# Performance work log

Measured on AMD Instinct MI355X. Metric: run time of the kernel, lower is better.

Reference implementation:

```python
import jax, jax.numpy as jnp
import numpy as np

N = 50000   # nodes
E = 800000  # edges (no self-loops; self-loops added in forward)
B = 128     # graphs
EPS = 1e-16  # PyG softmax denominator epsilon


def _gat(x, W, a_src, a_dst, bias, src, dst, heads, C, concat):
    n = x.shape[0]
    xp = (x @ W).reshape(n, heads, C)                      # [N,H,C]
    s_src = (xp * a_src).sum(-1)                           # [N,H]
    s_dst = (xp * a_dst).sum(-1)                           # [N,H]
    alpha = jax.nn.leaky_relu(s_src[src] + s_dst[dst], 0.2)  # [E',H]
    m = jax.ops.segment_max(alpha, dst, num_segments=n)
    ex = jnp.exp(alpha - m[dst])
    den = jax.ops.segment_sum(ex, dst, num_segments=n) + EPS
    a = ex / den[dst]                                      # edge softmax over in-edges
    out = jax.ops.segment_sum(a[:, :, None] * xp[src], dst, num_segments=n)  # [N,H,C]
    out = out.reshape(n, heads * C) if concat else out.mean(axis=1)
    return out + bias


def _forward(x, edge_attr, W1, b1, ln_g, ln_b, W2, b2,
             Wg1, as1, ad1, bg1, Wg2, as2, ad2, bg2, Wg3, as3, ad3, bg3,
             Wih, Whh, bih, bhh, edge_index, batch):
    # feature encoder: Linear -> LayerNorm -> LeakyReLU(0.1) -> Linear (dropout: eval mode)
    h = x @ W1 + b1
    mu = h.mean(-1, keepdims=True)
    var = ((h - mu) ** 2).mean(-1, keepdims=True)
    h = (h - mu) / jnp.sqrt(var + 1e-5) * ln_g + ln_b
    h = jax.nn.leaky_relu(h, 0.1)
    h = h @ W2 + b2                                        # [N,256]
    # add self loops once (edge_attr is unused: edge_dim=None => lin_edge is None)
    sl = jnp.arange(N, dtype=edge_index.dtype)
    src = jnp.concatenate([edge_index[0], sl])
    dst = jnp.concatenate([edge_index[1], sl])
    g = _gat(h, Wg1, as1, ad1, bg1, src, dst, 2, 64, True)   # [N,128]
    g = jax.nn.leaky_relu(g, 0.1)
    g = _gat(g, Wg2, as2, ad2, bg2, src, dst, 2, 64, True)   # [N,128]
    g = jax.nn.elu(g)
    g = _gat(g, Wg3, as3, ad3, bg3, src, dst, 1, 64, False)  # [N,64]
    # Set2Set(64, processing_steps=5)
    q_star = jnp.zeros((B, 128), g.dtype)
    hS = jnp.zeros((B, 64), g.dtype)
    cS = jnp.zeros((B, 64), g.dtype)
    for _ in range(5):
        gates = q_star @ Wih.T + bih + hS @ Whh.T + bhh      # [B,256]
        i, f, gg, o = jnp.split(gates, 4, axis=-1)
        cS = jax.nn.sigmoid(f) * cS + jax.nn.sigmoid(i) * jnp.tanh(gg)
        hS = jax.nn.sigmoid(o) * jnp.tanh(cS)                # q = h [B,64]
        e = (g * hS[batch]).sum(-1)                          # [N]
        m = jax.ops.segment_max(e, batch, num_segments=B)
        a = jnp.exp(e - m[batch])
        a = a / (jax.ops.segment_sum(a, batch, num_segments=B) + EPS)[batch]
        r = jax.ops.segment_sum(a[:, None] * g, batch, num_segments=B)  # [B,64]
        q_star = jnp.concatenate([hS, r], axis=-1)
    return q_star  # [B,128]


def setup_inputs():
    key = jax.random.key(0)
    ks = jax.random.split(key, 32)
    nrm = lambda k, sh, s=0.1: (jax.random.normal(k, sh) * s).astype(jnp.float32)
    src = jax.random.randint(ks[0], (E,), 0, N, dtype=jnp.int32)
    off = jax.random.randint(ks[1], (E,), 1, N, dtype=jnp.int32)
    dst = (src + off) % N  # no self-loops
    edge_index = jnp.stack([src, dst])
    batch = jnp.sort(jax.random.randint(ks[2], (N,), 0, B, dtype=jnp.int32))
    return dict(
        x=jax.random.normal(ks[3], (N, 6), jnp.float32),
        edge_index=edge_index,
        edge_attr=jax.random.normal(ks[4], (E, 4), jnp.float32),
        batch=batch,
        W1=nrm(ks[5], (6, 128)), b1=jnp.zeros((128,), jnp.float32),
        ln_g=jnp.ones((128,), jnp.float32), ln_b=jnp.zeros((128,), jnp.float32),
        W2=nrm(ks[6], (128, 256)), b2=jnp.zeros((256,), jnp.float32),
        Wg1=nrm(ks[7], (256, 128)), as1=nrm(ks[8], (2, 64)), ad1=nrm(ks[9], (2, 64)), bg1=jnp.zeros((128,), jnp.float32),
        Wg2=nrm(ks[10], (128, 128)), as2=nrm(ks[11], (2, 64)), ad2=nrm(ks[12], (2, 64)), bg2=jnp.zeros((128,), jnp.float32),
        Wg3=nrm(ks[13], (128, 64)), as3=nrm(ks[14], (1, 64)), ad3=nrm(ks[15], (1, 64)), bg3=jnp.zeros((64,), jnp.float32),
        Wih=nrm(ks[16], (256, 128)), Whh=nrm(ks[17], (256, 64)),
        bih=jnp.zeros((256,), jnp.float32), bhh=jnp.zeros((256,), jnp.float32),
    )


def reference(x, edge_index, edge_attr, batch, W1, b1, ln_g, ln_b, W2, b2,
              Wg1, as1, ad1, bg1, Wg2, as2, ad2, bg2, Wg3, as3, ad3, bg3,
              Wih, Whh, bih, bhh):
    return _forward(x, edge_attr, W1, b1, ln_g, ln_b, W2, b2,
                    Wg1, as1, ad1, bg1, Wg2, as2, ad2, bg2, Wg3, as3, ad3, bg3,
                    Wih, Whh, bih, bhh, edge_index, batch)
```

## Files before the change

### kernel.cpp

```cpp
#include <hip/hip_runtime.h>
#include <hip/hip_bf16.h>
#include <math.h>

#define N_NODES 50000
#define M_PAD   50176
#define N_EDGES 800000
#define N_B     128
#define EPRIME  (N_EDGES + N_NODES)
#define NBUCKETS 196
#define CCHUNK  8192
#define NCHUNKS ((EPRIME + CCHUNK - 1) / CCHUNK)
#define ENC_B   ((N_NODES + 3) / 4)
#define WT_B    (90112 / 256)
#define S2S_MAXN 512
#define GEMME_B  1564
#define GEMM1_B  782

typedef __attribute__((ext_vector_type(8))) short bf16x8;
typedef __attribute__((ext_vector_type(4))) float f32x4;
typedef unsigned short ushort_t;

__device__ __forceinline__ float sigmoidf_(float x) { return 1.f / (1.f + __expf(-x)); }

__device__ __forceinline__ void wtr1(const float* W, __hip_bfloat16* Wt, int K, int N, int i) {
    int k = i / N, n = i - k * N;
    Wt[(size_t)n * K + k] = __float2bfloat16(W[i]);
}

__global__ __launch_bounds__(256) void prep_k(
        const float* __restrict__ x, const float* __restrict__ W1,
        const float* __restrict__ b1, const float* __restrict__ lng,
        const float* __restrict__ lnb, __hip_bfloat16* __restrict__ h1,
        const float* __restrict__ W2, const float* __restrict__ Wg1,
        const float* __restrict__ Wg2, const float* __restrict__ Wg3,
        __hip_bfloat16* W2t, __hip_bfloat16* Wg1t,
        __hip_bfloat16* Wg2t, __hip_bfloat16* Wg3t,
        const int* __restrict__ e_dst, int* __restrict__ bpart) {
    int blk = blockIdx.x;
    if (blk < ENC_B) {
        int w = (blk * 256 + threadIdx.x) >> 6;
        int lane = threadIdx.x & 63;
        if (w >= N_NODES) return;
        float xr[6];
#pragma unroll
        for (int k = 0; k < 6; ++k) xr[k] = x[w * 6 + k];
        float a = b1[lane], b = b1[lane + 64];
#pragma unroll
        for (int k = 0; k < 6; ++k) {
            a += xr[k] * W1[k * 128 + lane];
            b += xr[k] * W1[k * 128 + 64 + lane];
        }
        float s = a + b, s2 = a * a + b * b;
        for (int o = 32; o; o >>= 1) { s += __shfl_xor(s, o); s2 += __shfl_xor(s2, o); }
        float mu  = s * (1.f / 128.f);
        float var = s2 * (1.f / 128.f) - mu * mu;
        float inv = rsqrtf(var + 1e-5f);
        a = (a - mu) * inv * lng[lane] + lnb[lane];
        b = (b - mu) * inv * lng[lane + 64] + lnb[lane + 64];
        a = a > 0.f ? a : 0.1f * a;
        b = b > 0.f ? b : 0.1f * b;
        h1[(size_t)w * 128 + lane]      = __float2bfloat16(a);
        h1[(size_t)w * 128 + 64 + lane] = __float2bfloat16(b);
    } else if (blk < ENC_B + WT_B) {
        int i = (blk - ENC_B) * 256 + threadIdx.x;
        if (i < 32768)       wtr1(W2,  W2t,  128, 256, i);
        else if (i < 65536)  wtr1(Wg1, Wg1t, 256, 128, i - 32768);
        else if (i < 81920)  wtr1(Wg2, Wg2t, 128, 128, i - 65536);
        else                 wtr1(Wg3, Wg3t, 128, 64,  i - 81920);
    } else {
        __shared__ int h[NBUCKETS];
        int c = blk - ENC_B - WT_B;
        for (int i = threadIdx.x; i < NBUCKETS; i += 256) h[i] = 0;
        __syncthreads();
        int base = c * CCHUNK;
        int end = min(base + CCHUNK, EPRIME);
        for (int e = base + threadIdx.x; e < end; e += 256) {
            int d = (e < N_EDGES) ? e_dst[e] : (e - N_EDGES);
            atomicAdd(&h[d >> 8], 1);
        }
        __syncthreads();
        for (int i = threadIdx.x; i < NBUCKETS; i += 256)
            bpart[c * NBUCKETS + i] = h[i];
    }
}

__global__ __launch_bounds__(256) void scan2_k(const int* __restrict__ bpart,
        int* __restrict__ boff, int* __restrict__ cpre) {
    __shared__ int sm[256];
    int t = threadIdx.x;
    int run = 0;
    if (t < NBUCKETS) {
        for (int j = 0; j < NCHUNKS; ++j) {
            cpre[j * NBUCKETS + t] = run;
            run += bpart[j * NBUCKETS + t];
        }
    }
    sm[t] = run; __syncthreads();
    for (int o = 1; o < 256; o <<= 1) {
        int xv = (t >= o) ? sm[t - o] : 0;
        __syncthreads();
        sm[t] += xv;
        __syncthreads();
    }
    int excl = sm[t] - run;
    if (t < NBUCKETS) boff[t] = excl;
    if (t == NBUCKETS - 1) boff[NBUCKETS] = excl + run;
}

__device__ __forceinline__ void partition_body(int c, const int* __restrict__ e_src,
        const int* __restrict__ e_dst, const int* __restrict__ boff,
        const int* __restrict__ cpre, int* __restrict__ epack,
        int* h2, int* gbase) {
    for (int i = threadIdx.x; i < NBUCKETS; i += 256) {
        h2[i] = 0;
        gbase[i] = boff[i] + cpre[c * NBUCKETS + i];
    }
    __syncthreads();
    int base = c * CCHUNK;
    int end = min(base + CCHUNK, EPRIME);
    for (int e = base + threadIdx.x; e < end; e += 256) {
        int s, d;
        if (e < N_EDGES) { s = e_src[e]; d = e_dst[e]; }
        else             { s = e - N_EDGES; d = s; }
        int b = d >> 8;
        int rank = atomicAdd(&h2[b], 1);
        epack[gbase[b] + rank] = ((d & 255) << 16) | s;
    }
}

__device__ __forceinline__ void csr_build_body(int b, const int* __restrict__ epack,
        const int* __restrict__ boff, int* __restrict__ off,
        ushort_t* __restrict__ csr, int* deg, int* cur, int* sm) {
    int t = threadIdx.x;
    int gb0 = boff[b];
    int gcnt = boff[b + 1] - gb0;
    deg[t] = 0;
    __syncthreads();
    for (int i = t; i < gcnt; i += 256)
        atomicAdd(&deg[(epack[gb0 + i] >> 16) & 0xFF], 1);
    __syncthreads();
    int v = deg[t];
    sm[t] = v; __syncthreads();
    for (int o = 1; o < 256; o <<= 1) {
        int xv = (t >= o) ? sm[t - o] : 0;
        __syncthreads();
        sm[t] += xv;
        __syncthreads();
    }
    int excl = sm[t] - v;
    int idx = b * 256 + t;
    if (idx <= N_NODES) off[idx] = gb0 + excl;
    cur[t] = gb0 + excl;
    __syncthreads();
    for (int i = t; i < gcnt; i += 256) {
        int pk = epack[gb0 + i];
        int ld = (pk >> 16) & 0xFF;
        int pos = atomicAdd(&cur[ld], 1);
        csr[pos] = (ushort_t)(pk & 0xFFFF);
    }
}

template<int K, int N, int BM, int BN, int WN, bool BIAS, int SDH>
__device__ __forceinline__ void mfma_body(short* As, float* sdbuf, int bx, int by,
        const __hip_bfloat16* __restrict__ A, const __hip_bfloat16* __restrict__ Wt,
        const float* __restrict__ bias, void* __restrict__ Cv,
        const float* __restrict__ asrc, const float* __restrict__ adst,
        float* __restrict__ ssrc, float* __restrict__ sdst, int M) {
    constexpr int KT = K / 32;
    constexpr int NISSUE = BM / 64;
    const int tid  = threadIdx.x;
    const int wid  = tid >> 6;
    const int lane = tid & 63;
    const int wm = wid / WN;
    const int wn = wid % WN;
    const int row0 = by * BM;
    const int col0 = bx * BN + wn * 32;

    if (SDH > 0) {
        for (int i = tid; i < BM * SDH * 2; i += 256) sdbuf[i] = 0.f;
    }

    bf16x8 breg[KT][2];
#pragma unroll
    for (int kt = 0; kt < KT; ++kt)
#pragma unroll
        for (int cb = 0; cb < 2; ++cb) {
            int col = col0 + cb * 16 + (lane & 15);
            int k   = kt * 32 + (lane >> 4) * 8;
            breg[kt][cb] = *(const bf16x8*)&Wt[(size_t)col * K + k];
        }

    f32x4 acc[4][2];
#pragma unroll
    for (int rb = 0; rb < 4; ++rb)
#pragma unroll
        for (int cb = 0; cb < 2; ++cb) acc[rb][cb] = f32x4{0.f, 0.f, 0.f, 0.f};

    int4 rbuf[NISSUE];
#pragma unroll
    for (int is = 0; is < NISSUE; ++is) {
        int lr = is * 64 + wid * 16 + (lane >> 2);
        rbuf[is] = *(const int4*)&A[(size_t)(row0 + lr) * K + (lane & 3) * 8];
    }
#pragma unroll
    for (int kt = 0; kt < KT; ++kt) {
        if (kt) __syncthreads();
#pragma unroll
        for (int is = 0; is < NISSUE; ++is) {
            int lr   = is * 64 + wid * 16 + (lane >> 2);
            int slot = (lane & 3) ^ ((lr >> 1) & 3);
            *(int4*)((char*)As + lr * 64 + slot * 16) = rbuf[is];
        }
        if (kt + 1 < KT) {
#pragma unroll
            for (int is = 0; is < NISSUE; ++is) {
                int lr = is * 64 + wid * 16 + (lane >> 2);
                rbuf[is] = *(const int4*)&A[(size_t)(row0 + lr) * K +
                                            (kt + 1) * 32 + (lane & 3) * 8];
            }
        }
        __syncthreads();
        bf16x8 af[4];
#pragma unroll
        for (int rb = 0; rb < 4; ++rb) {
            int row  = wm * 64 + rb * 16 + (lane & 15);
            int slot = (lane >> 4) ^ ((row >> 1) & 3);
            af[rb] = *(const bf16x8*)((char*)As + row * 64 + slot * 16);
        }
#pragma unroll
        for (int rb = 0; rb < 4; ++rb)
#pragma unroll
            for (int cb = 0; cb < 2; ++cb)
                acc[rb][cb] = __builtin_amdgcn_mfma_f32_16x16x32_bf16(
                    af[rb], breg[kt][cb], acc[rb][cb], 0, 0, 0);
    }

    if (SDH > 0) {
        float av0 = asrc[col0 + (lane & 15)],       ad0 = adst[col0 + (lane & 15)];
        float av1 = asrc[col0 + 16 + (lane & 15)],  ad1 = adst[col0 + 16 + (lane & 15)];
        int h = (SDH == 2) ? (wn >> 1) : 0;
#pragma unroll
        for (int rb = 0; rb < 4; ++rb) {
#pragma unroll
            for (int r = 0; r < 4; ++r) {
                float ssv = acc[rb][0][r] * av0 + acc[rb][1][r] * av1;
                float sdv = acc[rb][0][r] * ad0 + acc[rb][1][r] * ad1;
#pragma unroll
                for (int o = 1; o < 16; o <<= 1) {
                    ssv += __shfl_xor(ssv, o);
                    sdv += __shfl_xor(sdv, o);
                }
                if ((lane & 15) == 0) {
                    int rl = wm * 64 + rb * 16 + (lane >> 4) * 4 + r;
                    atomicAdd(&sdbuf[(rl * SDH + h) * 2 + 0], ssv);
                    atomicAdd(&sdbuf[(rl * SDH + h) * 2 + 1], sdv);
                }
            }
        }
        __syncthreads();
        if (tid < BM) {
            int row = row0 + tid;
            if (row < M) {
                if (SDH == 2) {
                    ((float2*)ssrc)[row] = make_float2(sdbuf[(tid * 2 + 0) * 2 + 0],
                                                       sdbuf[(tid * 2 + 1) * 2 + 0]);
                    ((float2*)sdst)[row] = make_float2(sdbuf[(tid * 2 + 0) * 2 + 1],
                                                       sdbuf[(tid * 2 + 1) * 2 + 1]);
                } else {
                    ssrc[row] = sdbuf[tid * 2 + 0];
                    sdst[row] = sdbuf[tid * 2 + 1];
                }
            }
        }
    }

#pragma unroll
    for (int rb = 0; rb < 4; ++rb) {
        int rowb = row0 + wm * 64 + rb * 16 + (lane >> 4) * 4;
#pragma unroll
        for (int cb = 0; cb < 2; ++cb) {
            int col = col0 + cb * 16 + (lane & 15);
            float bval = BIAS ? bias[col] : 0.f;
#pragma unroll
            for (int r = 0; r < 4; ++r) {
                int row = rowb + r;
                if (row < M) {
                    float v = acc[rb][cb][r] + bval;
                    ((__hip_bfloat16*)Cv)[(size_t)row * N + col] = __float2bfloat16(v);
                }
            }
        }
    }
}

__global__ __launch_bounds__(256) void gemmE_part_k(
        const __hip_bfloat16* __restrict__ A, const __hip_bfloat16* __restrict__ Wt,
        const float* __restrict__ bias, __hip_bfloat16* __restrict__ C,
        const int* __restrict__ e_src, const int* __restrict__ e_dst,
        const int* __restrict__ boff, const int* __restrict__ cpre,
        int* __restrict__ epack) {
    __shared__ short As[64 * 32];
    __shared__ int h2[NBUCKETS], gbase[NBUCKETS];
    int blk = blockIdx.x;
    if (blk < GEMME_B) {
        mfma_body<128, 256, 64, 128, 4, true, 0>(As, nullptr, blk & 1, blk >> 1,
            A, Wt, bias, C, nullptr, nullptr, nullptr, nullptr, N_NODES);
    } else {
        partition_body(blk - GEMME_B, e_src, e_dst, boff, cpre, epack, h2, gbase);
    }
}

__global__ __launch_bounds__(256) void gemm1_csr_k(
        const __hip_bfloat16* __restrict__ A, const __hip_bfloat16* __restrict__ Wt,
        __hip_bfloat16* __restrict__ C,
        const float* __restrict__ asrc, const float* __restrict__ adst,
        float* __restrict__ ssrc, float* __restrict__ sdst,
        const int* __restrict__ epack, const int* __restrict__ boff,
        int* __restrict__ off, ushort_t* __restrict__ csr) {
    __shared__ short As[64 * 32];
    __shared__ float sdbuf[64 * 2 * 2];
    __shared__ int deg[256], cur[256], sm[256];
    int blk = blockIdx.x;
    if (blk < GEMM1_B) {
        mfma_body<256, 128, 64, 128, 4, false, 2>(As, sdbuf, 0, blk,
            A, Wt, nullptr, C, asrc, adst, ssrc, sdst, N_NODES);
    } else {
        csr_build_body(blk - GEMM1_B, epack, boff, off, csr, deg, cur, sm);
    }
}

template<int K, int N, int BM, int BN, int WN, int SDH>
__global__ __launch_bounds__(256) void gemm_k(
        const __hip_bfloat16* __restrict__ A, const __hip_bfloat16* __restrict__ Wt,
        __hip_bfloat16* __restrict__ C,
        const float* __restrict__ asrc, const float* __restrict__ adst,
        float* __restrict__ ssrc, float* __restrict__ sdst) {
    __shared__ short As[BM * 32];
    __shared__ float sdbuf[SDH > 0 ? BM * SDH * 2 : 1];
    mfma_body<K, N, BM, BN, WN, false, SDH>(As, sdbuf, 0, blockIdx.x,
        A, Wt, nullptr, C, asrc, adst, ssrc, sdst, N_NODES);
}

template<int ACT>
__global__ __launch_bounds__(256) void gat_agg2_k(const __hip_bfloat16* __restrict__ xp,
        const float2* __restrict__ s_src2, const float2* __restrict__ s_dst2,
        const int* __restrict__ off, const ushort_t* __restrict__ csr_src,
        const float* __restrict__ bias, __hip_bfloat16* __restrict__ outb) {
    int n = (blockIdx.x * 256 + threadIdx.x) >> 6;
    int lane = threadIdx.x & 63;
    if (n >= N_NODES) return;
    const float2 sdn = s_dst2[n];
    const int i0 = off[n];
    const int deg = off[n + 1] - i0;
    const unsigned* __restrict__ xprow = (const unsigned*)xp;
    float accx = 0.f, accy = 0.f;
    float d0 = 0.f, d1 = 0.f;
    for (int c0 = 0; c0 < deg; c0 += 64) {
        int cnt = min(64, deg - c0);
        int se = 0; float e0 = 0.f, e1 = 0.f;
        if (lane < cnt) {
            se = csr_src[i0 + c0 + lane];
            float2 ssv = s_src2[se];
            float a0 = ssv.x + sdn.x; a0 = a0 > 0.f ? a0 : 0.2f * a0;
            float a1 = ssv.y + sdn.y; a1 = a1 > 0.f ? a1 : 0.2f * a1;
            e0 = __expf(a0); e1 = __expf(a1);
        }
        d0 += e0; d1 += e1;
        unsigned e0u = __float_as_uint(e0), e1u = __float_as_uint(e1);
        int e = 0;
        for (; e + 4 <= cnt; e += 4) {
            int s0 = __builtin_amdgcn_readlane(se, e + 0);
            int s1 = __builtin_amdgcn_readlane(se, e + 1);
            int s2 = __builtin_amdgcn_readlane(se, e + 2);
            int s3 = __builtin_amdgcn_readlane(se, e + 3);
            unsigned w0 = xprow[((unsigned)s0 << 6) + lane];
            unsigned w1 = xprow[((unsigned)s1 << 6) + lane];
            unsigned w2 = xprow[((unsigned)s2 << 6) + lane];
            unsigned w3 = xprow[((unsigned)s3 << 6) + lane];
            float p00 = __uint_as_float(__builtin_amdgcn_readlane(e0u, e + 0));
            float p01 = __uint_as_float(__builtin_amdgcn_readlane(e1u, e + 0));
            float p10 = __uint_as_float(__builtin_amdgcn_readlane(e0u, e + 1));
            float p11 = __uint_as_float(__builtin_amdgcn_readlane(e1u, e + 1));
            float p20 = __uint_as_float(__builtin_amdgcn_readlane(e0u, e + 2));
            float p21 = __uint_as_float(__builtin_amdgcn_readlane(e1u, e + 2));
            float p30 = __uint_as_float(__builtin_amdgcn_readlane(e0u, e + 3));
            float p31 = __uint_as_float(__builtin_amdgcn_readlane(e1u, e + 3));
            float q0 = lane < 32 ? p00 : p01;
            float q1 = lane < 32 ? p10 : p11;
            float q2 = lane < 32 ? p20 : p21;
            float q3 = lane < 32 ? p30 : p31;
            accx += q0 * __uint_as_float(w0 << 16);
            accy += q0 * __uint_as_float(w0 & 0xffff0000u);
            accx += q1 * __uint_as_float(w1 << 16);
            accy += q1 * __uint_as_float(w1 & 0xffff0000u);
            accx += q2 * __uint_as_float(w2 << 16);
            accy += q2 * __uint_as_float(w2 & 0xffff0000u);
            accx += q3 * __uint_as_float(w3 << 16);
            accy += q3 * __uint_as_float(w3 & 0xffff0000u);
        }
        for (; e < cnt; ++e) {
            int s = __builtin_amdgcn_readlane(se, e);
            unsigned w = xprow[((unsigned)s << 6) + lane];
            float p0 = __uint_as_float(__builtin_amdgcn_readlane(e0u, e));
            float p1 = __uint_as_float(__builtin_amdgcn_readlane(e1u, e));
            float q = lane < 32 ? p0 : p1;
            accx += q * __uint_as_float(w << 16);
            accy += q * __uint_as_float(w & 0xffff0000u);
        }
    }
    for (int o = 32; o; o >>= 1) { d0 += __shfl_xor(d0, o); d1 += __shfl_xor(d1, o); }
    float den = (lane < 32 ? d0 : d1) + 1e-16f;
    float2 bv = ((const float2*)bias)[lane];
    float r0 = accx / den + bv.x;
    float r1 = accy / den + bv.y;
    if (ACT == 1) { r0 = r0 > 0.f ? r0 : 0.1f * r0; r1 = r1 > 0.f ? r1 : 0.1f * r1; }
    else          { r0 = r0 > 0.f ? r0 : (__expf(r0) - 1.f);
                    r1 = r1 > 0.f ? r1 : (__expf(r1) - 1.f); }
    __hip_bfloat16 h0 = __float2bfloat16(r0), h1v = __float2bfloat16(r1);
    unsigned packed = (unsigned)*(unsigned short*)&h0 |
                      ((unsigned)*(unsigned short*)&h1v << 16);
    ((unsigned*)outb)[(size_t)n * 64 + lane] = packed;
}

__global__ __launch_bounds__(256) void gat_agg1_k(const __hip_bfloat16* __restrict__ xp,
        const float* __restrict__ s_src, const float* __restrict__ s_dst,
        const int* __restrict__ off, const ushort_t* __restrict__ csr_src,
        const float* __restrict__ bias, float* __restrict__ out) {
    int n = (blockIdx.x * 256 + threadIdx.x) >> 6;
    int lane = threadIdx.x & 63;
    if (n >= N_NODES) return;
    const float sdn = s_dst[n];
    const int i0 = off[n];
    const int deg = off[n + 1] - i0;
    float acc = 0.f, d0 = 0.f;
    for (int c0 = 0; c0 < deg; c0 += 64) {
        int cnt = min(64, deg - c0);
        int se = 0; float ev = 0.f;
        if (lane < cnt) {
            se = csr_src[i0 + c0 + lane];
            float a = s_src[se] + sdn;
            a = a > 0.f ? a : 0.2f * a;
            ev = __expf(a);
        }
        d0 += ev;
        unsigned evu = __float_as_uint(ev);
        int e = 0;
        for (; e + 4 <= cnt; e += 4) {
            int s0 = __builtin_amdgcn_readlane(se, e + 0);
            int s1 = __builtin_amdgcn_readlane(se, e + 1);
            int s2 = __builtin_amdgcn_readlane(se, e + 2);
            int s3 = __builtin_amdgcn_readlane(se, e + 3);
            float w0 = __uint_as_float(__builtin_amdgcn_readlane(evu, e + 0));
            float w1 = __uint_as_float(__builtin_amdgcn_readlane(evu, e + 1));
            float w2 = __uint_as_float(__builtin_amdgcn_readlane(evu, e + 2));
            float w3 = __uint_as_float(__builtin_amdgcn_readlane(evu, e + 3));
            acc += w0 * __bfloat162float(xp[((unsigned)s0 << 6) + lane]);
            acc += w1 * __bfloat162float(xp[((unsigned)s1 << 6) + lane]);
            acc += w2 * __bfloat162float(xp[((unsigned)s2 << 6) + lane]);
            acc += w3 * __bfloat162float(xp[((unsigned)s3 << 6) + lane]);
        }
        for (; e < cnt; ++e) {
            int s = __builtin_amdgcn_readlane(se, e);
            float w = __uint_as_float(__builtin_amdgcn_readlane(evu, e));
            acc += w * __bfloat162float(xp[((unsigned)s << 6) + lane]);
        }
    }
    for (int o = 32; o; o >>= 1) d0 += __shfl_xor(d0, o);
    out[(size_t)n * 64 + lane] = acc / (d0 + 1e-16f) + bias[lane];
}

__global__ __launch_bounds__(512) void s2s_fused_k(const float* __restrict__ g3,
        const int* __restrict__ batch,
        const float* __restrict__ Wih, const float* __restrict__ Whh,
        const float* __restrict__ bih, const float* __restrict__ bhh,
        float* __restrict__ out) {
    __shared__ __align__(16) float g3L[S2S_MAXN * 68];
    __shared__ float p_sh[S2S_MAXN];
    __shared__ __align__(16) float hsh[64];
    __shared__ float q[128], csh[64], gates[256];
    __shared__ float rred[8][64];
    __shared__ float dred[8];
    __shared__ int sn0, sn1;
    int b = blockIdx.x;
    int t = threadIdx.x;
    int lane = t & 63, wv = t >> 6;
    if (t == 0) {
        int lo = 0, hi = N_NODES;
        while (lo < hi) { int mid = (lo + hi) >> 1; if (batch[mid] < b) lo = mid + 1; else hi = mid; }
        sn0 = lo;
        lo = 0; hi = N_NODES;
        while (lo < hi) { int mid = (lo + hi) >> 1; if (batch[mid] < b + 1) lo = mid + 1; else hi = mid; }
        sn1 = lo;
    }
    if (t < 128) q[t] = 0.f;
    if (t < 64) { hsh[t] = 0.f; csh[t] = 0.f; }
    __syncthreads();
    const int n0 = sn0;
    const int cnt = min(sn1 - sn0, S2S_MAXN);
    for (int i = t; i < cnt * 16; i += 512) {
        int r = i >> 4, c4 = i & 15;
        ((float4*)&g3L[r * 68])[c4] = ((const float4*)(g3 + ((size_t)(n0 + r) << 6)))[c4];
    }
    __syncthreads();
    for (int step = 0; step < 5; ++step) {
        if (t < 256) {
            float g = bih[t] + bhh[t];
            const float4* wi4 = (const float4*)(Wih + (size_t)t * 128);
#pragma unroll 8
            for (int k4 = 0; k4 < 32; ++k4) {
                float4 w = wi4[k4];
                g += q[k4 * 4 + 0] * w.x + q[k4 * 4 + 1] * w.y +
                     q[k4 * 4 + 2] * w.z + q[k4 * 4 + 3] * w.w;
            }
            const float4* wh4 = (const float4*)(Whh + (size_t)t * 64);
#pragma unroll 8
            for (int k4 = 0; k4 < 16; ++k4) {
                float4 w = wh4[k4];
                g += hsh[k4 * 4 + 0] * w.x + hsh[k4 * 4 + 1] * w.y +
                     hsh[k4 * 4 + 2] * w.z + hsh[k4 * 4 + 3] * w.w;
            }
            gates[t] = g;
        }
        __syncthreads();
        if (t < 64) {
            float iv = sigmoidf_(gates[t]);
            float fv = sigmoidf_(gates[64 + t]);
            float gv = tanhf(gates[128 + t]);
            float ov = sigmoidf_(gates[192 + t]);
            float c = fv * csh[t] + iv * gv;
            csh[t] = c;
            hsh[t] = ov * tanhf(c);
        }
        __syncthreads();
        float4 hr[16];
#pragma unroll
        for (int k = 0; k < 16; ++k) hr[k] = ((const float4*)hsh)[k];
        for (int base = 0; base < cnt; base += 512) {
            int n = base + t;
            if (n < cnt) {
                const float4* row = (const float4*)&g3L[n * 68];
                float a0 = 0.f, a1 = 0.f, a2 = 0.f, a3 = 0.f;
#pragma unroll
                for (int k = 0; k < 16; k += 4) {
                    float4 r0 = row[k], r1 = row[k + 1], r2 = row[k + 2], r3 = row[k + 3];
                    a0 += r0.x * hr[k].x + r0.y * hr[k].y + r0.z * hr[k].z + r0.w * hr[k].w;
                    a1 += r1.x * hr[k+1].x + r1.y * hr[k+1].y + r1.z * hr[k+1].z + r1.w * hr[k+1].w;
                    a2 += r2.x * hr[k+2].x + r2.y * hr[k+2].y + r2.z * hr[k+2].z + r2.w * hr[k+2].w;
                    a3 += r3.x * hr[k+3].x + r3.y * hr[k+3].y + r3.z * hr[k+3].z + r3.w * hr[k+3].w;
                }
                p_sh[n] = __expf((a0 + a1) + (a2 + a3));
            }
        }
        __syncthreads();
        float rloc = 0.f, dloc = 0.f;
        int n = wv;
        for (; n + 8 < cnt; n += 16) {
            float pv0 = p_sh[n], pv1 = p_sh[n + 8];
            float gv0 = g3L[n * 68 + lane], gv1 = g3L[(n + 8) * 68 + lane];
            dloc += pv0 + pv1;
            rloc += pv0 * gv0 + pv1 * gv1;
        }
        if (n < cnt) {
            float pv = p_sh[n];
            float gv = g3L[n * 68 + lane];
            dloc += pv; rloc += pv * gv;
        }
        rred[wv][lane] = rloc;
        if (lane == 0) dred[wv] = dloc;
        __syncthreads();
        if (t < 64) {
            float r = rred[0][t] + rred[1][t] + rred[2][t] + rred[3][t] +
                      rred[4][t] + rred[5][t] + rred[6][t] + rred[7][t];
            float den = dred[0] + dred[1] + dred[2] + dred[3] +
                        dred[4] + dred[5] + dred[6] + dred[7] + 1e-16f;
            q[t] = hsh[t];
            q[64 + t] = r / den;
        }
        __syncthreads();
    }
    if (t < 128) out[b * 128 + t] = q[t];
}

extern "C" void kernel_launch(void* const* d_in, const int* in_sizes, int n_in,
                              void* d_out, int out_size, void* d_ws, size_t ws_size,
                              hipStream_t stream) {
    (void)in_sizes; (void)n_in; (void)out_size; (void)ws_size;
    const float* x     = (const float*)d_in[0];
    const int*   ei    = (const int*)d_in[1];
    const int*   batch = (const int*)d_in[3];
    const float* W1  = (const float*)d_in[4];
    const float* b1  = (const float*)d_in[5];
    const float* lng = (const float*)d_in[6];
    const float* lnb = (const float*)d_in[7];
    const float* W2  = (const float*)d_in[8];
    const float* b2  = (const float*)d_in[9];
    const float* Wg1 = (const float*)d_in[10];
    const float* as1 = (const float*)d_in[11];
    const float* ad1 = (const float*)d_in[12];
    const float* bg1 = (const float*)d_in[13];
    const float* Wg2 = (const float*)d_in[14];
    const float* as2 = (const float*)d_in[15];
    const float* ad2 = (const float*)d_in[16];
    const float* bg2 = (const float*)d_in[17];
    const float* Wg3 = (const float*)d_in[18];
    const float* as3 = (const float*)d_in[19];
    const float* ad3 = (const float*)d_in[20];
    const float* bg3 = (const float*)d_in[21];
    const float* Wih = (const float*)d_in[22];
    const float* Whh = (const float*)d_in[23];
    const float* bih = (const float*)d_in[24];
    const float* bhh = (const float*)d_in[25];
    const int* e_src = ei;
    const int* e_dst = ei + N_EDGES;
    float* out = (float*)d_out;

    char* p = (char*)d_ws;
    auto carve = [&](size_t bytes) {
        char* r = p;
        p += (bytes + 255) & ~(size_t)255;
        return r;
    };
    __hip_bfloat16* actA = (__hip_bfloat16*)carve((size_t)M_PAD * 256 * 2);
    __hip_bfloat16* actB = (__hip_bfloat16*)carve((size_t)M_PAD * 128 * 2);
    __hip_bfloat16* actC = (__hip_bfloat16*)carve((size_t)M_PAD * 128 * 2);
    float* g3     = (float*)carve((size_t)M_PAD * 64 * 4);
    float* s_src  = (float*)carve((size_t)N_NODES * 2 * 4);
    float* s_dst  = (float*)carve((size_t)N_NODES * 2 * 4);
    int*   off    = (int*)carve((size_t)(N_NODES + 1) * 4);
    int*   epack  = (int*)carve((size_t)EPRIME * 4);
    ushort_t* csr = (ushort_t*)carve((size_t)EPRIME * 2);
    int*   bpart  = (int*)carve((size_t)NCHUNKS * NBUCKETS * 4);
    int*   cpre   = (int*)carve((size_t)NCHUNKS * NBUCKETS * 4);
    int*   boff   = (int*)carve((NBUCKETS + 1) * 4);
    __hip_bfloat16* W2t  = (__hip_bfloat16*)carve(256 * 128 * 2);
    __hip_bfloat16* Wg1t = (__hip_bfloat16*)carve(128 * 256 * 2);
    __hip_bfloat16* Wg2t = (__hip_bfloat16*)carve(128 * 128 * 2);
    __hip_bfloat16* Wg3t = (__hip_bfloat16*)carve(64 * 128 * 2);

    dim3 blk(256);

    prep_k<<<ENC_B + WT_B + NCHUNKS, blk, 0, stream>>>(
        x, W1, b1, lng, lnb, actB,
        W2, Wg1, Wg2, Wg3, W2t, Wg1t, Wg2t, Wg3t,
        e_dst, bpart);

    scan2_k<<<1, blk, 0, stream>>>(bpart, boff, cpre);

    gemmE_part_k<<<GEMME_B + NCHUNKS, blk, 0, stream>>>(
        actB, W2t, b2, actA, e_src, e_dst, boff, cpre, epack);

    gemm1_csr_k<<<GEMM1_B + NBUCKETS, blk, 0, stream>>>(
        actA, Wg1t, actB, as1, ad1, s_src, s_dst, epack, boff, off, csr);
    gat_agg2_k<1><<<(N_NODES + 3) / 4, blk, 0, stream>>>(
        actB, (const float2*)s_src, (const float2*)s_dst, off, csr, bg1, actC);

    gemm_k<128, 128, 64, 128, 4, 2><<<GEMM1_B, blk, 0, stream>>>(
        actC, Wg2t, actB, as2, ad2, s_src, s_dst);
    gat_agg2_k<2><<<(N_NODES + 3) / 4, blk, 0, stream>>>(
        actB, (const float2*)s_src, (const float2*)s_dst, off, csr, bg2, actC);

    gemm_k<128, 64, 128, 64, 2, 1><<<391, blk, 0, stream>>>(
        actC, Wg3t, actB, as3, ad3, s_src, s_dst);
    gat_agg1_k<<<(N_NODES + 3) / 4, blk, 0, stream>>>(
        actB, s_src, s_dst, off, csr, bg3, g3);

    s2s_fused_k<<<N_B, dim3(512), 0, stream>>>(g3, batch, Wih, Whh, bih, bhh, out);
}
```

Measured before the change: 398.2 us.

## Gather neighbor rows with 16-byte loads per edge group and transpose LSTM weights

```diff
diff --git a/kernel.cpp b/kernel.cpp
--- a/kernel.cpp
+++ b/kernel.cpp
@@ -11,7 +11,8 @@
 #define CCHUNK  8192
 #define NCHUNKS ((EPRIME + CCHUNK - 1) / CCHUNK)
 #define ENC_B   ((N_NODES + 3) / 4)
-#define WT_B    (90112 / 256)
+#define WT_ELEMS (90112 + 32768 + 16384)
+#define WT_B    ((WT_ELEMS + 255) / 256)
 #define S2S_MAXN 512
 #define GEMME_B  1564
 #define GEMM1_B  782
@@ -35,6 +36,8 @@
         const float* __restrict__ Wg2, const float* __restrict__ Wg3,
         __hip_bfloat16* W2t, __hip_bfloat16* Wg1t,
         __hip_bfloat16* Wg2t, __hip_bfloat16* Wg3t,
+        const float* __restrict__ Wih, const float* __restrict__ Whh,
+        float* __restrict__ WihT, float* __restrict__ WhhT,
         const int* __restrict__ e_dst, int* __restrict__ bpart) {
     int blk = blockIdx.x;
     if (blk < ENC_B) {
@@ -66,7 +69,16 @@
         if (i < 32768)       wtr1(W2,  W2t,  128, 256, i);
         else if (i < 65536)  wtr1(Wg1, Wg1t, 256, 128, i - 32768);
         else if (i < 81920)  wtr1(Wg2, Wg2t, 128, 128, i - 65536);
-        else                 wtr1(Wg3, Wg3t, 128, 64,  i - 81920);
+        else if (i < 90112)  wtr1(Wg3, Wg3t, 128, 64,  i - 81920);
+        else if (i < 122880) {
+            int ii = i - 90112;
+            int k = ii >> 8, j = ii & 255;
+            WihT[ii] = Wih[(size_t)j * 128 + k];
+        } else if (i < WT_ELEMS) {
+            int ii = i - 122880;
+            int k = ii >> 8, j = ii & 255;
+            WhhT[ii] = Whh[(size_t)j * 64 + k];
+        }
     } else {
         __shared__ int h[NBUCKETS];
         int c = blk - ENC_B - WT_B;
@@ -349,12 +361,15 @@
     int n = (blockIdx.x * 256 + threadIdx.x) >> 6;
     int lane = threadIdx.x & 63;
     if (n >= N_NODES) return;
+    const int grp = lane >> 4;
+    const int slot = lane & 15;
     const float2 sdn = s_dst2[n];
     const int i0 = off[n];
     const int deg = off[n + 1] - i0;
-    const unsigned* __restrict__ xprow = (const unsigned*)xp;
-    float accx = 0.f, accy = 0.f;
+    const int4* __restrict__ xprow4 = (const int4*)xp;
+    float acc[8] = {0.f, 0.f, 0.f, 0.f, 0.f, 0.f, 0.f, 0.f};
     float d0 = 0.f, d1 = 0.f;
+    const int bbase = grp << 2;
     for (int c0 = 0; c0 < deg; c0 += 64) {
         int cnt = min(64, deg - c0);
         int se = 0; float e0 = 0.f, e1 = 0.f;
@@ -366,60 +381,54 @@
             e0 = __expf(a0); e1 = __expf(a1);
         }
         d0 += e0; d1 += e1;
-        unsigned e0u = __float_as_uint(e0), e1u = __float_as_uint(e1);
-        int e = 0;
-        for (; e + 4 <= cnt; e += 4) {
-            int s0 = __builtin_amdgcn_readlane(se, e + 0);
-            int s1 = __builtin_amdgcn_readlane(se, e + 1);
-            int s2 = __builtin_amdgcn_readlane(se, e + 2);
-            int s3 = __builtin_amdgcn_readlane(se, e + 3);
-            unsigned w0 = xprow[((unsigned)s0 << 6) + lane];
-            unsigned w1 = xprow[((unsigned)s1 << 6) + lane];
-            unsigned w2 = xprow[((unsigned)s2 << 6) + lane];
-            unsigned w3 = xprow[((unsigned)s3 << 6) + lane];
-            float p00 = __uint_as_float(__builtin_amdgcn_readlane(e0u, e + 0));
-            float p01 = __uint_as_float(__builtin_amdgcn_readlane(e1u, e + 0));
-            float p10 = __uint_as_float(__builtin_amdgcn_readlane(e0u, e + 1));
-            float p11 = __uint_as_float(__builtin_amdgcn_readlane(e1u, e + 1));
-            float p20 = __uint_as_float(__builtin_amdgcn_readlane(e0u, e + 2));
-            float p21 = __uint_as_float(__builtin_amdgcn_readlane(e1u, e + 2));
-            float p30 = __uint_as_float(__builtin_amdgcn_readlane(e0u, e + 3));
-            float p31 = __uint_as_float(__builtin_amdgcn_readlane(e1u, e + 3));
-            float q0 = lane < 32 ? p00 : p01;
-            float q1 = lane < 32 ? p10 : p11;
-            float q2 = lane < 32 ? p20 : p21;
-            float q3 = lane < 32 ? p30 : p31;
-            accx += q0 * __uint_as_float(w0 << 16);
-            accy += q0 * __uint_as_float(w0 & 0xffff0000u);
-            accx += q1 * __uint_as_float(w1 << 16);
-            accy += q1 * __uint_as_float(w1 & 0xffff0000u);
-            accx += q2 * __uint_as_float(w2 << 16);
-            accy += q2 * __uint_as_float(w2 & 0xffff0000u);
-            accx += q3 * __uint_as_float(w3 << 16);
-            accy += q3 * __uint_as_float(w3 & 0xffff0000u);
-        }
-        for (; e < cnt; ++e) {
-            int s = __builtin_amdgcn_readlane(se, e);
-            unsigned w = xprow[((unsigned)s << 6) + lane];
-            float p0 = __uint_as_float(__builtin_amdgcn_readlane(e0u, e));
-            float p1 = __uint_as_float(__builtin_amdgcn_readlane(e1u, e));
-            float q = lane < 32 ? p0 : p1;
-            accx += q * __uint_as_float(w << 16);
-            accy += q * __uint_as_float(w & 0xffff0000u);
-        }
+        int e0i = __float_as_int(e0), e1i = __float_as_int(e1);
+        for (int e = 0; e < cnt; e += 4) {
+            int bidx = (e << 2) + bbase;
+            int s  = __builtin_amdgcn_ds_bpermute(bidx, se);
+            float w0 = __int_as_float(__builtin_amdgcn_ds_bpermute(bidx, e0i));
+            float w1 = __int_as_float(__builtin_amdgcn_ds_bpermute(bidx, e1i));
+            float qv = slot < 8 ? w0 : w1;
+            int4 row = xprow4[(size_t)s * 16 + slot];
+            acc[0] += qv * __uint_as_float((unsigned)row.x << 16);
+            acc[1] += qv * __uint_as_float((unsigned)row.x & 0xffff0000u);
+            acc[2] += qv * __uint_as_float((unsigned)row.y << 16);
+            acc[3] += qv * __uint_as_float((unsigned)row.y & 0xffff0000u);
+            acc[4] += qv * __uint_as_float((unsigned)row.z << 16);
+            acc[5] += qv * __uint_as_float((unsigned)row.z & 0xffff0000u);
+            acc[6] += qv * __uint_as_float((unsigned)row.w << 16);
+            acc[7] += qv * __uint_as_float((unsigned)row.w & 0xffff0000u);
+        }
+    }
+#pragma unroll
+    for (int j = 0; j < 8; ++j) {
+        acc[j] += __shfl_xor(acc[j], 16);
+        acc[j] += __shfl_xor(acc[j], 32);
     }
     for (int o = 32; o; o >>= 1) { d0 += __shfl_xor(d0, o); d1 += __shfl_xor(d1, o); }
-    float den = (lane < 32 ? d0 : d1) + 1e-16f;
-    float2 bv = ((const float2*)bias)[lane];
-    float r0 = accx / den + bv.x;
-    float r1 = accy / den + bv.y;
-    if (ACT == 1) { r0 = r0 > 0.f ? r0 : 0.1f * r0; r1 = r1 > 0.f ? r1 : 0.1f * r1; }
-    else          { r0 = r0 > 0.f ? r0 : (__expf(r0) - 1.f);
-                    r1 = r1 > 0.f ? r1 : (__expf(r1) - 1.f); }
-    __hip_bfloat16 h0 = __float2bfloat16(r0), h1v = __float2bfloat16(r1);
-    unsigned packed = (unsigned)*(unsigned short*)&h0 |
-                      ((unsigned)*(unsigned short*)&h1v << 16);
-    ((unsigned*)outb)[(size_t)n * 64 + lane] = packed;
+    if (grp == 0) {
+        float den = (slot < 8 ? d0 : d1) + 1e-16f;
+        float4 bv0 = ((const float4*)bias)[slot * 2];
+        float4 bv1 = ((const float4*)bias)[slot * 2 + 1];
+        float r[8];
+        r[0] = acc[0] / den + bv0.x; r[1] = acc[1] / den + bv0.y;
+        r[2] = acc[2] / den + bv0.z; r[3] = acc[3] / den + bv0.w;
+        r[4] = acc[4] / den + bv1.x; r[5] = acc[5] / den + bv1.y;
+        r[6] = acc[6] / den + bv1.z; r[7] = acc[7] / den + bv1.w;
+#pragma unroll
+        for (int j = 0; j < 8; ++j) {
+            if (ACT == 1) r[j] = r[j] > 0.f ? r[j] : 0.1f * r[j];
+            else          r[j] = r[j] > 0.f ? r[j] : (__expf(r[j]) - 1.f);
+        }
+        int pk[4];
+#pragma unroll
+        for (int j = 0; j < 4; ++j) {
+            __hip_bfloat16 lo = __float2bfloat16(r[2 * j]);
+            __hip_bfloat16 hi = __float2bfloat16(r[2 * j + 1]);
+            pk[j] = (int)(unsigned)*(unsigned short*)&lo |
+                    ((int)(unsigned)*(unsigned short*)&hi << 16);
+        }
+        ((int4*)outb)[(size_t)n * 16 + slot] = make_int4(pk[0], pk[1], pk[2], pk[3]);
+    }
 }
 
 __global__ __launch_bounds__(256) void gat_agg1_k(const __hip_bfloat16* __restrict__ xp,
@@ -429,10 +438,15 @@
     int n = (blockIdx.x * 256 + threadIdx.x) >> 6;
     int lane = threadIdx.x & 63;
     if (n >= N_NODES) return;
+    const int grp = lane >> 3;
+    const int slot = lane & 7;
     const float sdn = s_dst[n];
     const int i0 = off[n];
     const int deg = off[n + 1] - i0;
-    float acc = 0.f, d0 = 0.f;
+    const int4* __restrict__ xprow4 = (const int4*)xp;
+    float acc[8] = {0.f, 0.f, 0.f, 0.f, 0.f, 0.f, 0.f, 0.f};
+    float d0 = 0.f;
+    const int bbase = grp << 2;
     for (int c0 = 0; c0 < deg; c0 += 64) {
         int cnt = min(64, deg - c0);
         int se = 0; float ev = 0.f;
@@ -443,41 +457,52 @@
             ev = __expf(a);
         }
         d0 += ev;
-        unsigned evu = __float_as_uint(ev);
-        int e = 0;
-        for (; e + 4 <= cnt; e += 4) {
-            int s0 = __builtin_amdgcn_readlane(se, e + 0);
-            int s1 = __builtin_amdgcn_readlane(se, e + 1);
-            int s2 = __builtin_amdgcn_readlane(se, e + 2);
-            int s3 = __builtin_amdgcn_readlane(se, e + 3);
-            float w0 = __uint_as_float(__builtin_amdgcn_readlane(evu, e + 0));
-            float w1 = __uint_as_float(__builtin_amdgcn_readlane(evu, e + 1));
-            float w2 = __uint_as_float(__builtin_amdgcn_readlane(evu, e + 2));
-            float w3 = __uint_as_float(__builtin_amdgcn_readlane(evu, e + 3));
-            acc += w0 * __bfloat162float(xp[((unsigned)s0 << 6) + lane]);
-            acc += w1 * __bfloat162float(xp[((unsigned)s1 << 6) + lane]);
-            acc += w2 * __bfloat162float(xp[((unsigned)s2 << 6) + lane]);
-            acc += w3 * __bfloat162float(xp[((unsigned)s3 << 6) + lane]);
-        }
-        for (; e < cnt; ++e) {
-            int s = __builtin_amdgcn_readlane(se, e);
-            float w = __uint_as_float(__builtin_amdgcn_readlane(evu, e));
-            acc += w * __bfloat162float(xp[((unsigned)s << 6) + lane]);
-        }
+        int evi = __float_as_int(ev);
+        for (int e = 0; e < cnt; e += 8) {
+            int bidx = (e << 2) + bbase;
+            int s  = __builtin_amdgcn_ds_bpermute(bidx, se);
+            float qv = __int_as_float(__builtin_amdgcn_ds_bpermute(bidx, evi));
+            int4 row = xprow4[(size_t)s * 8 + slot];
+            acc[0] += qv * __uint_as_float((unsigned)row.x << 16);
+            acc[1] += qv * __uint_as_float((unsigned)row.x & 0xffff0000u);
+            acc[2] += qv * __uint_as_float((unsigned)row.y << 16);
+            acc[3] += qv * __uint_as_float((unsigned)row.y & 0xffff0000u);
+            acc[4] += qv * __uint_as_float((unsigned)row.z << 16);
+            acc[5] += qv * __uint_as_float((unsigned)row.z & 0xffff0000u);
+            acc[6] += qv * __uint_as_float((unsigned)row.w << 16);
+            acc[7] += qv * __uint_as_float((unsigned)row.w & 0xffff0000u);
+        }
+    }
+#pragma unroll
+    for (int j = 0; j < 8; ++j) {
+        acc[j] += __shfl_xor(acc[j], 8);
+        acc[j] += __shfl_xor(acc[j], 16);
+        acc[j] += __shfl_xor(acc[j], 32);
     }
     for (int o = 32; o; o >>= 1) d0 += __shfl_xor(d0, o);
-    out[(size_t)n * 64 + lane] = acc / (d0 + 1e-16f) + bias[lane];
+    if (grp == 0) {
+        float den = d0 + 1e-16f;
+        float4 bv0 = ((const float4*)bias)[slot * 2];
+        float4 bv1 = ((const float4*)bias)[slot * 2 + 1];
+        float4 r0 = make_float4(acc[0] / den + bv0.x, acc[1] / den + bv0.y,
+                                acc[2] / den + bv0.z, acc[3] / den + bv0.w);
+        float4 r1 = make_float4(acc[4] / den + bv1.x, acc[5] / den + bv1.y,
+                                acc[6] / den + bv1.z, acc[7] / den + bv1.w);
+        ((float4*)out)[(size_t)n * 16 + slot * 2]     = r0;
+        ((float4*)out)[(size_t)n * 16 + slot * 2 + 1] = r1;
+    }
 }
 
 __global__ __launch_bounds__(512) void s2s_fused_k(const float* __restrict__ g3,
         const int* __restrict__ batch,
-        const float* __restrict__ Wih, const float* __restrict__ Whh,
+        const float* __restrict__ WihT, const float* __restrict__ WhhT,
         const float* __restrict__ bih, const float* __restrict__ bhh,
         float* __restrict__ out) {
     __shared__ __align__(16) float g3L[S2S_MAXN * 68];
     __shared__ float p_sh[S2S_MAXN];
     __shared__ __align__(16) float hsh[64];
-    __shared__ float q[128], csh[64], gates[256];
+    __shared__ float q[128], csh[64];
+    __shared__ float gA[256], gB[256];
     __shared__ float rred[8][64];
     __shared__ float dred[8];
     __shared__ int sn0, sn1;
@@ -504,29 +529,23 @@
     __syncthreads();
     for (int step = 0; step < 5; ++step) {
         if (t < 256) {
-            float g = bih[t] + bhh[t];
-            const float4* wi4 = (const float4*)(Wih + (size_t)t * 128);
+            float g = 0.f;
 #pragma unroll 8
-            for (int k4 = 0; k4 < 32; ++k4) {
-                float4 w = wi4[k4];
-                g += q[k4 * 4 + 0] * w.x + q[k4 * 4 + 1] * w.y +
-                     q[k4 * 4 + 2] * w.z + q[k4 * 4 + 3] * w.w;
-            }
-            const float4* wh4 = (const float4*)(Whh + (size_t)t * 64);
+            for (int k = 0; k < 128; ++k) g += q[k] * WihT[k * 256 + t];
+            gA[t] = g;
+        } else {
+            int j = t - 256;
+            float g = bih[j] + bhh[j];
 #pragma unroll 8
-            for (int k4 = 0; k4 < 16; ++k4) {
-                float4 w = wh4[k4];
-                g += hsh[k4 * 4 + 0] * w.x + hsh[k4 * 4 + 1] * w.y +
-                     hsh[k4 * 4 + 2] * w.z + hsh[k4 * 4 + 3] * w.w;
-            }
-            gates[t] = g;
+            for (int k = 0; k < 64; ++k) g += hsh[k] * WhhT[k * 256 + j];
+            gB[j] = g;
         }
         __syncthreads();
         if (t < 64) {
-            float iv = sigmoidf_(gates[t]);
-            float fv = sigmoidf_(gates[64 + t]);
-            float gv = tanhf(gates[128 + t]);
-            float ov = sigmoidf_(gates[192 + t]);
+            float iv = sigmoidf_(gA[t] + gB[t]);
+            float fv = sigmoidf_(gA[64 + t] + gB[64 + t]);
+            float gv = tanhf(gA[128 + t] + gB[128 + t]);
+            float ov = sigmoidf_(gA[192 + t] + gB[192 + t]);
             float c = fv * csh[t] + iv * gv;
             csh[t] = c;
             hsh[t] = ov * tanhf(c);
@@ -636,12 +655,15 @@
     __hip_bfloat16* Wg1t = (__hip_bfloat16*)carve(128 * 256 * 2);
     __hip_bfloat16* Wg2t = (__hip_bfloat16*)carve(128 * 128 * 2);
     __hip_bfloat16* Wg3t = (__hip_bfloat16*)carve(64 * 128 * 2);
+    float* WihT = (float*)carve(128 * 256 * 4);
+    float* WhhT = (float*)carve(64 * 256 * 4);
 
     dim3 blk(256);
 
     prep_k<<<ENC_B + WT_B + NCHUNKS, blk, 0, stream>>>(
         x, W1, b1, lng, lnb, actB,
         W2, Wg1, Wg2, Wg3, W2t, Wg1t, Wg2t, Wg3t,
+        Wih, Whh, WihT, WhhT,
         e_dst, bpart);
 
     scan2_k<<<1, blk, 0, stream>>>(bpart, boff, cpre);
@@ -664,5 +686,5 @@
     gat_agg1_k<<<(N_NODES + 3) / 4, blk, 0, stream>>>(
         actB, s_src, s_dst, off, csr, bg3, g3);
 
-    s2s_fused_k<<<N_B, dim3(512), 0, stream>>>(g3, batch, Wih, Whh, bih, bhh, out);
-}
+    s2s_fused_k<<<N_B, dim3(512), 0, stream>>>(g3, batch, WihT, WhhT, bih, bhh, out);
+}
```

Result: no change. 391.7 us (-1.6%).
